# Optimization experiments

Hardware: AMD Instinct MI355X
Metric: run time of the kernel (lower is better)

## Reference

```python
import jax, jax.numpy as jnp
import numpy as np
from jax import lax

B, C, H, W = 4, 256, 64, 64
R = 4  # reduction
BN_EPS = 1e-5


def setup_inputs() -> dict:
    key = jax.random.key(0)
    ks = jax.random.split(key, 18)
    n = jax.random.normal
    return {
        "x_self": n(ks[0], (B, C, H, W), jnp.float32),
        "x_other": n(ks[1], (B, C, H, W), jnp.float32),
        "q_w": n(ks[2], (C, C), jnp.float32) * 0.05,      # self_q 1x1 conv
        "q_b": n(ks[3], (C,), jnp.float32) * 0.05,
        "kv_w": n(ks[4], (2 * C, C), jnp.float32) * 0.05,  # other_kv 1x1 conv
        "kv_b": n(ks[5], (2 * C,), jnp.float32) * 0.05,
        "g1_w": n(ks[6], (C // R, C), jnp.float32) * 0.05,  # gate conv1
        "g1_b": n(ks[7], (C // R,), jnp.float32) * 0.05,
        "g2_w": n(ks[8], (1, C // R), jnp.float32) * 0.05,  # gate conv2
        "g2_b": n(ks[9], (1,), jnp.float32) * 0.05,
        "dw_w": n(ks[10], (C, 1, 3, 3), jnp.float32) * 0.1,  # depthwise 3x3
        "dw_b": n(ks[11], (C,), jnp.float32) * 0.05,
        "bn_g": jnp.ones((C,), jnp.float32),
        "bn_b": jnp.zeros((C,), jnp.float32),
        "bn_m": n(ks[12], (C,), jnp.float32) * 0.05,
        "bn_v": jax.random.uniform(ks[13], (C,), jnp.float32, 0.5, 1.5),
        "out_w": n(ks[14], (C, C), jnp.float32) * 0.05,
        "out_b": n(ks[15], (C,), jnp.float32) * 0.05,
    }


def _conv1x1(x, w, b):
    return jnp.einsum('bchw,oc->bohw', x, w) + b[None, :, None, None]


def reference(x_self, x_other, q_w, q_b, kv_w, kv_b, g1_w, g1_b, g2_w, g2_b,
              dw_w, dw_b, bn_g, bn_b, bn_m, bn_v, out_w, out_b):
    # local branch: depthwise 3x3 conv -> BatchNorm (eval stats) -> SiLU
    y = lax.conv_general_dilated(
        x_self, dw_w, (1, 1), 'SAME',
        feature_group_count=C,
        dimension_numbers=('NCHW', 'OIHW', 'NCHW')) + dw_b[None, :, None, None]
    scale = (bn_g / jnp.sqrt(bn_v + BN_EPS))[None, :, None, None]
    y = (y - bn_m[None, :, None, None]) * scale + bn_b[None, :, None, None]
    local_feat = y * jax.nn.sigmoid(y)  # SiLU

    # cross attention over HW tokens
    q = _conv1x1(x_self, q_w, q_b).reshape(B, C, H * W)
    kv = _conv1x1(x_other, kv_w, kv_b)
    k = kv[:, :C].reshape(B, C, H * W)
    v = kv[:, C:].reshape(B, C, H * W)
    attn = jnp.einsum('bcn,bcm->bnm', q, k) / jnp.sqrt(jnp.float32(C))  # [B,HW,HW]
    attn = jax.nn.softmax(attn, axis=-1)
    attn_out = jnp.einsum('bnm,bcm->bcn', attn, v).reshape(B, C, H, W)

    # channel-squeeze gate on x_self -> scalar per sample
    p = jnp.mean(x_self, axis=(2, 3))                 # [B,C] global avg pool
    g = jax.nn.relu(p @ g1_w.T + g1_b)                # [B,C//R]
    g = jax.nn.sigmoid(g @ g2_w.T + g2_b)             # [B,1]
    gate = g[:, :, None, None]

    fused = local_feat + gate * attn_out
    return _conv1x1(fused, out_w, out_b)
```

## Files before the change

kernel.cpp:

```cpp
#include <hip/hip_runtime.h>
#include <stdint.h>

#define BB 4
#define CC 256
#define HH 64
#define WWD 64
#define NN 4096
#define LOG2E 1.4426950408889634f

typedef __attribute__((ext_vector_type(8))) short short8;
typedef __attribute__((ext_vector_type(4))) float f32x4;
typedef __attribute__((ext_vector_type(16))) float f32x16;
typedef __attribute__((ext_vector_type(4))) unsigned short us4;

__device__ __forceinline__ unsigned short f2bf(float f) {
  unsigned int u = __float_as_uint(f);
  u += 0x7fffu + ((u >> 16) & 1u);
  return (unsigned short)(u >> 16);
}
__device__ __forceinline__ float bf2f(unsigned short h) {
  return __uint_as_float(((unsigned int)h) << 16);
}
__device__ __forceinline__ short8 ld8(const unsigned short* p) {
  return *reinterpret_cast<const short8*>(p);
}
__device__ __forceinline__ int rowmap(int reg, int h) {
  return (reg & 3) + 8 * (reg >> 2) + 4 * h;
}

__global__ __launch_bounds__(256, 2) void k_pre(
    const float* __restrict__ xs, const float* __restrict__ xo,
    const float* __restrict__ dww, const float* __restrict__ dwb,
    const float* __restrict__ bng, const float* __restrict__ bnb,
    const float* __restrict__ bnm, const float* __restrict__ bnv,
    const float* __restrict__ qw, const float* __restrict__ kvw,
    const float* __restrict__ ow, unsigned short* __restrict__ XtS,
    unsigned short* __restrict__ XtO, unsigned short* __restrict__ localT,
    float* __restrict__ psumA, unsigned short* __restrict__ Wb) {
  __shared__ float rb3[3][64][67];
  __shared__ unsigned short sb[64][67];
  int tid = threadIdx.x;
  if (blockIdx.z == 8) {
    int i = (blockIdx.x * 64 + blockIdx.y) * 1024 + tid * 4;
    const float* src;
    if (i < 65536) src = qw + i;
    else if (i < 196608) src = kvw + (i - 65536);
    else src = ow + (i - 196608);
    f32x4 v = *reinterpret_cast<const f32x4*>(src);
    us4 r;
#pragma unroll
    for (int j = 0; j < 4; ++j) r[j] = f2bf(v[j]);
    *reinterpret_cast<us4*>(Wb + i) = r;
    return;
  }
  int c0 = blockIdx.x * 64, h = blockIdx.y;
  int b = blockIdx.z >> 1, which = blockIdx.z & 1;
  const float* src = which ? xo : xs;
  int wq = tid >> 6, w = tid & 63;
  int dlo = which ? 1 : 0, dhi = which ? 1 : 2;
  for (int d = dlo; d <= dhi; ++d) {
    int hh = h + d - 1;
    bool ok = (hh >= 0 && hh < HH);
    for (int p = 0; p < 16; ++p) {
      int cl = p * 4 + wq;
      rb3[d][cl][w + 1] =
          ok ? src[(((size_t)(b * CC + c0 + cl)) * HH + hh) * WWD + w] : 0.f;
    }
    if (tid < 64) { rb3[d][tid][0] = 0.f; rb3[d][tid][65] = 0.f; }
  }
  __syncthreads();
  unsigned short* dst = which ? XtO : XtS;
  int n0 = h * 64, cb = (tid & 15) * 4;
#pragma unroll
  for (int i = 0; i < 4; ++i) {
    int wl = i * 16 + (tid >> 4);
    us4 r;
#pragma unroll
    for (int j = 0; j < 4; ++j) r[j] = f2bf(rb3[1][cb + j][wl + 1]);
    *reinterpret_cast<us4*>(&dst[((size_t)b * NN + n0 + wl) * CC + c0 + cb]) = r;
  }
  if (which) return;
  if (tid < 64) {
    float s = 0.f;
    for (int ww = 0; ww < 64; ++ww) s += rb3[1][tid][ww + 1];
    psumA[((size_t)(b * 64 + h)) * CC + c0 + tid] = s;
  }
  for (int p = 0; p < 16; ++p) {
    int cl = p * 4 + wq, c = c0 + cl;
    float acc = 0.f;
#pragma unroll
    for (int di = 0; di < 3; ++di)
#pragma unroll
      for (int dj = 0; dj < 3; ++dj)
        acc = fmaf(rb3[di][cl][w + dj], dww[c * 9 + di * 3 + dj], acc);
    float y = acc + dwb[c];
    float sc = bng[c] * rsqrtf(bnv[c] + 1e-5f);
    float v = (y - bnm[c]) * sc + bnb[c];
    sb[cl][w] = f2bf(v / (1.f + __expf(-v)));
  }
  __syncthreads();
#pragma unroll
  for (int i = 0; i < 4; ++i) {
    int wl = i * 16 + (tid >> 4);
    us4 r;
#pragma unroll
    for (int j = 0; j < 4; ++j) r[j] = sb[cb + j][wl];
    *reinterpret_cast<us4*>(&localT[((size_t)b * NN + n0 + wl) * CC + c0 + cb]) = r;
  }
}

__global__ __launch_bounds__(256, 4) void k_qkv(
    const unsigned short* __restrict__ XtS, const unsigned short* __restrict__ XtO,
    const unsigned short* __restrict__ Wb, const float* __restrict__ qb,
    const float* __restrict__ kvb, const float* __restrict__ psumA,
    const float* __restrict__ g1w, const float* __restrict__ g1b,
    const float* __restrict__ g2w, const float* __restrict__ g2b,
    unsigned short* __restrict__ Qt, unsigned short* __restrict__ Kt,
    unsigned short* __restrict__ Vv, float* __restrict__ gate) {
  __shared__ unsigned short Xs[64][264];
  int tid = threadIdx.x;
  int id = blockIdx.y;
  if (id == 3) {
    if (blockIdx.x != 0 || blockIdx.z != 0) return;
    float* mf = (float*)&Xs[0][0];
    float* hpf = mf + 1024;
    int c = tid;
    for (int b4 = 0; b4 < 4; ++b4) {
      float s = 0.f;
      for (int hh = 0; hh < 64; ++hh) s += psumA[((size_t)(b4 * 64 + hh)) * CC + c];
      mf[b4 * 256 + c] = s * (1.f / 4096.f);
    }
    __syncthreads();
    for (int b4 = 0; b4 < 4; ++b4) {
      int j = tid >> 2, cq = tid & 3;
      float s = 0.f;
      for (int cc = cq * 64; cc < cq * 64 + 64; ++cc)
        s = fmaf(mf[b4 * 256 + cc], g1w[j * CC + cc], s);
      hpf[j * 5 + cq] = s;
      __syncthreads();
      if (tid < 64) {
        float hh = fmaxf(hpf[tid * 5] + hpf[tid * 5 + 1] + hpf[tid * 5 + 2] +
                             hpf[tid * 5 + 3] + g1b[tid], 0.f);
        float t = hh * g2w[tid];
        for (int off = 32; off; off >>= 1) t += __shfl_down(t, off, 64);
        if (tid == 0) gate[b4] = 1.f / (1.f + expf(-(t + g2b[0])));
      }
      __syncthreads();
    }
    return;
  }
  int n0 = blockIdx.x * 64, b = blockIdx.z;
  const unsigned short* Xt = (id == 0) ? XtS : XtO;
  const unsigned short* W = Wb + id * 65536;
  int wave = tid >> 6, lane = tid & 63, l31 = lane & 31, h = lane >> 5;
#pragma unroll
  for (int p = 0; p < 8; ++p) {
    int r = p * 8 + (tid >> 5), c = (tid & 31) * 8;
    *reinterpret_cast<uint4*>(&Xs[r][c]) =
        *reinterpret_cast<const uint4*>(Xt + ((size_t)b * NN + n0 + r) * CC + c);
  }
  __syncthreads();
  int o0 = wave * 64;
  f32x16 acc[4] = {};
  if (id < 2) {
#pragma unroll
    for (int t = 0; t < 16; ++t) {
      short8 a0 = ld8(&Xs[l31][t * 16 + h * 8]);
      short8 a1 = ld8(&Xs[32 + l31][t * 16 + h * 8]);
      short8 b0 = ld8(W + (size_t)(o0 + l31) * CC + t * 16 + h * 8);
      short8 b1 = ld8(W + (size_t)(o0 + 32 + l31) * CC + t * 16 + h * 8);
      acc[0] = __builtin_amdgcn_mfma_f32_32x32x16_bf16(a0, b0, acc[0], 0, 0, 0);
      acc[1] = __builtin_amdgcn_mfma_f32_32x32x16_bf16(a0, b1, acc[1], 0, 0, 0);
      acc[2] = __builtin_amdgcn_mfma_f32_32x32x16_bf16(a1, b0, acc[2], 0, 0, 0);
      acc[3] = __builtin_amdgcn_mfma_f32_32x32x16_bf16(a1, b1, acc[3], 0, 0, 0);
    }
    const float* bias = id ? kvb : qb;
    unsigned short* Out = id ? Kt : Qt;
    float scale = id ? 1.0f : 0.0625f;
#pragma unroll
    for (int nt = 0; nt < 2; ++nt)
#pragma unroll
      for (int ot = 0; ot < 2; ++ot) {
        int o = o0 + ot * 32 + l31;
        float bv = bias[o];
#pragma unroll
        for (int reg = 0; reg < 16; ++reg) {
          int n = n0 + nt * 32 + rowmap(reg, h);
          Out[((size_t)b * NN + n) * CC + o] = f2bf((acc[nt * 2 + ot][reg] + bv) * scale);
        }
      }
  } else {
#pragma unroll
    for (int t = 0; t < 16; ++t) {
      short8 a0 = ld8(W + (size_t)(o0 + l31) * CC + t * 16 + h * 8);
      short8 a1 = ld8(W + (size_t)(o0 + 32 + l31) * CC + t * 16 + h * 8);
      short8 b0 = ld8(&Xs[l31][t * 16 + h * 8]);
      short8 b1 = ld8(&Xs[32 + l31][t * 16 + h * 8]);
      acc[0] = __builtin_amdgcn_mfma_f32_32x32x16_bf16(a0, b0, acc[0], 0, 0, 0);
      acc[1] = __builtin_amdgcn_mfma_f32_32x32x16_bf16(a0, b1, acc[1], 0, 0, 0);
      acc[2] = __builtin_amdgcn_mfma_f32_32x32x16_bf16(a1, b0, acc[2], 0, 0, 0);
      acc[3] = __builtin_amdgcn_mfma_f32_32x32x16_bf16(a1, b1, acc[3], 0, 0, 0);
    }
#pragma unroll
    for (int ot = 0; ot < 2; ++ot)
#pragma unroll
      for (int nt = 0; nt < 2; ++nt)
#pragma unroll
        for (int reg = 0; reg < 16; ++reg) {
          int o = o0 + ot * 32 + rowmap(reg, h);
          int n = n0 + nt * 32 + l31;
          Vv[((size_t)b * CC + o) * NN + n] = f2bf(acc[ot * 2 + nt][reg] + kvb[CC + o]);
        }
  }
}

__global__ __launch_bounds__(256, 2) void k_flash2(
    const unsigned short* __restrict__ Qt, const unsigned short* __restrict__ Kt,
    const unsigned short* __restrict__ V, const unsigned short* __restrict__ localT,
    const float* __restrict__ gate, float* __restrict__ Opart, float* __restrict__ Lpart,
    unsigned short* __restrict__ fusedT, int iters) {
  __shared__ unsigned short Ks[64][264];
  __shared__ unsigned short Vs[256][72];
  __shared__ unsigned short Ps[64][72];
  __shared__ float lred[2][64];
  __shared__ float ltot[64];
  int b = blockIdx.x & 3, n0 = (blockIdx.x >> 2) * 64;
  int sp = blockIdx.y, nsp = gridDim.y;
  int tid = threadIdx.x, wave = tid >> 6, lane = tid & 63, l31 = lane & 31, h = lane >> 5;
  int rw = wave & 1, cw = wave >> 1;
  const unsigned short* qp = Qt + ((size_t)b * NN + n0 + rw * 32 + l31) * CC + h * 8;
  short8 qf[16];
#pragma unroll
  for (int t = 0; t < 16; ++t) qf[t] = ld8(qp + t * 16);
  f32x16 O[4] = {};
  float lacc[16] = {};
  int mbase = sp * iters * 64;
  for (int it = 0; it < iters; ++it) {
    int m0 = mbase + it * 64;
    __syncthreads();
#pragma unroll
    for (int p = 0; p < 8; ++p) {
      int m = p * 8 + (tid >> 5), ccol = (tid & 31) * 8;
      *reinterpret_cast<uint4*>(&Ks[m][ccol]) =
          *reinterpret_cast<const uint4*>(Kt + ((size_t)b * NN + m0 + m) * CC + ccol);
    }
#pragma unroll
    for (int p = 0; p < 8; ++p) {
      int ccol = p * 32 + (tid >> 3), mm = (tid & 7) * 8;
      *reinterpret_cast<uint4*>(&Vs[ccol][mm]) =
          *reinterpret_cast<const uint4*>(V + ((size_t)b * CC + ccol) * NN + m0 + mm);
    }
    __syncthreads();
    f32x16 S = {};
#pragma unroll
    for (int t = 0; t < 16; ++t) {
      short8 kf = ld8(&Ks[cw * 32 + l31][t * 16 + h * 8]);
      S = __builtin_amdgcn_mfma_f32_32x32x16_bf16(qf[t], kf, S, 0, 0, 0);
    }
#pragma unroll
    for (int reg = 0; reg < 16; ++reg) {
      float p = __builtin_exp2f(S[reg] * LOG2E);
      lacc[reg] += p;
      Ps[rw * 32 + rowmap(reg, h)][cw * 32 + l31] = f2bf(p);
    }
    __syncthreads();
#pragma unroll
    for (int t = 0; t < 4; ++t) {
      short8 pf = ld8(&Ps[rw * 32 + l31][t * 16 + h * 8]);
#pragma unroll
      for (int ct = 0; ct < 4; ++ct) {
        short8 vf = ld8(&Vs[cw * 128 + ct * 32 + l31][t * 16 + h * 8]);
        O[ct] = __builtin_amdgcn_mfma_f32_32x32x16_bf16(pf, vf, O[ct], 0, 0, 0);
      }
    }
  }
#pragma unroll
  for (int reg = 0; reg < 16; ++reg) {
    float v = lacc[reg];
#pragma unroll
    for (int msk = 1; msk < 32; msk <<= 1) v += __shfl_xor(v, msk, 64);
    lacc[reg] = v;
  }
  __syncthreads();
#pragma unroll
  for (int g = 0; g < 16; ++g)
    if (l31 == g) lred[cw][rw * 32 + rowmap(g, h)] = lacc[g];
  __syncthreads();
  size_t obase2 = (size_t)(b * nsp + sp) * NN;
  if (nsp == 1) {
    if (tid < 64) ltot[tid] = lred[0][tid] + lred[1][tid];
    __syncthreads();
    float gv = gate[b];
    float inv[16];
#pragma unroll
    for (int reg = 0; reg < 16; ++reg)
      inv[reg] = gv / ltot[rw * 32 + rowmap(reg, h)];
#pragma unroll
    for (int ct = 0; ct < 4; ++ct)
#pragma unroll
      for (int reg = 0; reg < 16; ++reg) {
        int n = n0 + rw * 32 + rowmap(reg, h);
        int c = cw * 128 + ct * 32 + l31;
        size_t idx = ((size_t)b * NN + n) * CC + c;
        fusedT[idx] = f2bf(bf2f(localT[idx]) + O[ct][reg] * inv[reg]);
      }
  } else {
    if (tid < 64) Lpart[obase2 + n0 + tid] = lred[0][tid] + lred[1][tid];
#pragma unroll
    for (int ct = 0; ct < 4; ++ct)
#pragma unroll
      for (int reg = 0; reg < 16; ++reg) {
        int n = n0 + rw * 32 + rowmap(reg, h);
        int c = cw * 128 + ct * 32 + l31;
        Opart[(obase2 + n) * CC + c] = O[ct][reg];
      }
  }
}

__global__ __launch_bounds__(256, 4) void k_out(
    const unsigned short* __restrict__ W, const float* __restrict__ ob,
    const float* __restrict__ gate, const unsigned short* __restrict__ localT,
    const float* __restrict__ Opart, const float* __restrict__ Lpart,
    const unsigned short* __restrict__ fusedT, float* __restrict__ out, int nsp) {
  __shared__ unsigned short Xs[64][264];
  int n0 = blockIdx.x * 64, o0 = blockIdx.y * 128, b = blockIdx.z;
  int tid = threadIdx.x, wave = tid >> 6, lane = tid & 63, l31 = lane & 31, h = lane >> 5;
  if (Opart) {
    float gv = gate[b];
#pragma unroll
    for (int p = 0; p < 8; ++p) {
      int r = p * 8 + (tid >> 5), cc = (tid & 31) * 8;
      int n = n0 + r;
      float lsum = 0.f;
      for (int sp = 0; sp < nsp; ++sp) lsum += Lpart[(size_t)(b * nsp + sp) * NN + n];
      float g = gv / lsum;
      f32x4 o0v = {}, o1v = {};
      for (int sp = 0; sp < nsp; ++sp) {
        const float* op = &Opart[((size_t)(b * nsp + sp) * NN + n) * CC + cc];
        o0v += *reinterpret_cast<const f32x4*>(op);
        o1v += *reinterpret_cast<const f32x4*>(op + 4);
      }
      const unsigned short* lp = localT + ((size_t)b * NN + n) * CC + cc;
      us4 l0 = *reinterpret_cast<const us4*>(lp), l1 = *reinterpret_cast<const us4*>(lp + 4);
      us4 r0, r1;
#pragma unroll
      for (int j = 0; j < 4; ++j) {
        r0[j] = f2bf(bf2f(l0[j]) + o0v[j] * g);
        r1[j] = f2bf(bf2f(l1[j]) + o1v[j] * g);
      }
      *reinterpret_cast<us4*>(&Xs[r][cc]) = r0;
      *reinterpret_cast<us4*>(&Xs[r][cc + 4]) = r1;
    }
  } else {
#pragma unroll
    for (int p = 0; p < 8; ++p) {
      int r = p * 8 + (tid >> 5), c = (tid & 31) * 8;
      *reinterpret_cast<uint4*>(&Xs[r][c]) =
          *reinterpret_cast<const uint4*>(fusedT + ((size_t)b * NN + n0 + r) * CC + c);
    }
  }
  int obase = o0 + wave * 32;
  short8 af[16];
#pragma unroll
  for (int t = 0; t < 16; ++t) af[t] = ld8(W + (size_t)(obase + l31) * CC + t * 16 + h * 8);
  __syncthreads();
  f32x16 acc[2] = {};
#pragma unroll
  for (int t = 0; t < 16; ++t) {
    short8 b0 = ld8(&Xs[l31][t * 16 + h * 8]);
    short8 b1 = ld8(&Xs[32 + l31][t * 16 + h * 8]);
    acc[0] = __builtin_amdgcn_mfma_f32_32x32x16_bf16(af[t], b0, acc[0], 0, 0, 0);
    acc[1] = __builtin_amdgcn_mfma_f32_32x32x16_bf16(af[t], b1, acc[1], 0, 0, 0);
  }
#pragma unroll
  for (int nt = 0; nt < 2; ++nt)
#pragma unroll
    for (int reg = 0; reg < 16; ++reg) {
      int o = obase + rowmap(reg, h);
      int n = n0 + nt * 32 + l31;
      out[((size_t)b * CC + o) * NN + n] = acc[nt][reg] + ob[o];
    }
}

extern "C" void kernel_launch(void* const* d_in, const int* in_sizes, int n_in,
                              void* d_out, int out_size, void* d_ws, size_t ws_size,
                              hipStream_t stream) {
  const float* xs  = (const float*)d_in[0];
  const float* xo  = (const float*)d_in[1];
  const float* qw  = (const float*)d_in[2];
  const float* qb  = (const float*)d_in[3];
  const float* kvw = (const float*)d_in[4];
  const float* kvb = (const float*)d_in[5];
  const float* g1w = (const float*)d_in[6];
  const float* g1b = (const float*)d_in[7];
  const float* g2w = (const float*)d_in[8];
  const float* g2b = (const float*)d_in[9];
  const float* dww = (const float*)d_in[10];
  const float* dwb = (const float*)d_in[11];
  const float* bng = (const float*)d_in[12];
  const float* bnb = (const float*)d_in[13];
  const float* bnm = (const float*)d_in[14];
  const float* bnv = (const float*)d_in[15];
  const float* ow  = (const float*)d_in[16];
  const float* ob  = (const float*)d_in[17];
  float* out = (float*)d_out;
  char* ws = (char*)d_ws;

  const size_t SZ = (size_t)BB * NN * CC * 2;
  unsigned short* XtS    = (unsigned short*)(ws);
  unsigned short* XtO    = (unsigned short*)(ws + SZ);
  unsigned short* Qt     = (unsigned short*)(ws + 2 * SZ);
  unsigned short* Kt     = (unsigned short*)(ws + 3 * SZ);
  unsigned short* Vv     = (unsigned short*)(ws + 4 * SZ);
  unsigned short* localT = (unsigned short*)(ws + 5 * SZ);
  unsigned short* Wb     = (unsigned short*)(ws + 6 * SZ);
  float* psumA = (float*)(ws + 6 * SZ + 524288);
  float* gate  = (float*)(ws + 6 * SZ + 524288 + 262144);
  size_t tail  = 6 * SZ + 524288 + 262144 + 4096;
  float* Lpart = (float*)(ws + tail);
  float* Opart = (float*)(ws + tail + 131072);
  unsigned short* fusedT = XtS;

  size_t need2 = tail + 131072 + 2ull * 16777216;
  int S = (ws_size >= need2) ? 2 : 1;

  k_pre<<<dim3(4, 64, 9), 256, 0, stream>>>(xs, xo, dww, dwb, bng, bnb, bnm, bnv,
                                            qw, kvw, ow, XtS, XtO, localT, psumA, Wb);
  k_qkv<<<dim3(64, 4, 4), 256, 0, stream>>>(XtS, XtO, Wb, qb, kvb, psumA,
                                            g1w, g1b, g2w, g2b, Qt, Kt, Vv, gate);
  k_flash2<<<dim3(256, S), 256, 0, stream>>>(Qt, Kt, Vv, localT, gate, Opart, Lpart,
                                             fusedT, 64 / S);
  k_out<<<dim3(64, 2, 4), 256, 0, stream>>>(Wb + 196608, ob, gate, localT,
                                            S > 1 ? Opart : nullptr, Lpart, fusedT,
                                            out, S);
}
```

Baseline: 282.8 us.

## Switch attention Q/K/V and P to FP8 MFMA with LDS-staged stores and 3-way split

Q, K, V are now produced as FP8 (with the 1/16 softmax scale split as 0.25 on each of Q and K), staged through shared memory for coalesced 16-byte global stores. The flash kernel uses FP8 32x32x16 MFMAs for both QK^T and PV with byte-sized LDS tiles, and writes bf16 partial outputs. The key split can go to 3 when the workspace allows. The input load in the prologue is also vectorised to float4. The aim is to halve attention memory traffic and speed up the MFMAs. In exchange, FP8 precision on the softmax probabilities and on Q/K/V risks accuracy loss against tolerance.

New measurement: 251.6 us. 11.0% less time.

```diff
diff --git a/kernel.cpp b/kernel.cpp
--- a/kernel.cpp
+++ b/kernel.cpp
@@ -12,6 +12,7 @@
 typedef __attribute__((ext_vector_type(4))) float f32x4;
 typedef __attribute__((ext_vector_type(16))) float f32x16;
 typedef __attribute__((ext_vector_type(4))) unsigned short us4;
+typedef unsigned long long ull;
 
 __device__ __forceinline__ unsigned short f2bf(float f) {
   unsigned int u = __float_as_uint(f);
@@ -23,6 +24,9 @@
 }
 __device__ __forceinline__ short8 ld8(const unsigned short* p) {
   return *reinterpret_cast<const short8*>(p);
+}
+__device__ __forceinline__ unsigned char f2fp8(float v) {
+  return (unsigned char)__builtin_amdgcn_cvt_pk_fp8_f32(v, v, 0, false);
 }
 __device__ __forceinline__ int rowmap(int reg, int h) {
   return (reg & 3) + 8 * (reg >> 2) + 4 * h;
@@ -61,10 +65,16 @@
   for (int d = dlo; d <= dhi; ++d) {
     int hh = h + d - 1;
     bool ok = (hh >= 0 && hh < HH);
-    for (int p = 0; p < 16; ++p) {
-      int cl = p * 4 + wq;
-      rb3[d][cl][w + 1] =
-          ok ? src[(((size_t)(b * CC + c0 + cl)) * HH + hh) * WWD + w] : 0.f;
+#pragma unroll
+    for (int p = 0; p < 4; ++p) {
+      int idx = p * 256 + tid;
+      int cl = idx >> 4, ws4 = (idx & 15) * 4;
+      f32x4 v = {};
+      if (ok)
+        v = *reinterpret_cast<const f32x4*>(
+            &src[(((size_t)(b * CC + c0 + cl)) * HH + hh) * WWD + ws4]);
+#pragma unroll
+      for (int j = 0; j < 4; ++j) rb3[d][cl][ws4 + 1 + j] = v[j];
     }
     if (tid < 64) { rb3[d][tid][0] = 0.f; rb3[d][tid][65] = 0.f; }
   }
@@ -105,7 +115,7 @@
     us4 r;
 #pragma unroll
     for (int j = 0; j < 4; ++j) r[j] = sb[cb + j][wl];
-    *reinterpret_cast<us4*>(&localT[((size_t)b * NN + n0 + wl) * CC + c0 + cb]) = r;
+    *reinterpret_cast<us4*>(&localT[((size_t)b * NN + h * WWD + wl) * CC + c0 + cb]) = r;
   }
 }
 
@@ -115,8 +125,8 @@
     const float* __restrict__ kvb, const float* __restrict__ psumA,
     const float* __restrict__ g1w, const float* __restrict__ g1b,
     const float* __restrict__ g2w, const float* __restrict__ g2b,
-    unsigned short* __restrict__ Qt, unsigned short* __restrict__ Kt,
-    unsigned short* __restrict__ Vv, float* __restrict__ gate) {
+    unsigned char* __restrict__ Qt8, unsigned char* __restrict__ Kt8,
+    unsigned char* __restrict__ Vv8, float* __restrict__ gate) {
   __shared__ unsigned short Xs[64][264];
   int tid = threadIdx.x;
   int id = blockIdx.y;
@@ -175,8 +185,9 @@
       acc[3] = __builtin_amdgcn_mfma_f32_32x32x16_bf16(a1, b1, acc[3], 0, 0, 0);
     }
     const float* bias = id ? kvb : qb;
-    unsigned short* Out = id ? Kt : Qt;
-    float scale = id ? 1.0f : 0.0625f;
+    unsigned char* Out8 = id ? Kt8 : Qt8;
+    __syncthreads();
+    unsigned char (*T8)[264] = reinterpret_cast<unsigned char(*)[264]>(&Xs[0][0]);
 #pragma unroll
     for (int nt = 0; nt < 2; ++nt)
 #pragma unroll
@@ -185,10 +196,21 @@
         float bv = bias[o];
 #pragma unroll
         for (int reg = 0; reg < 16; ++reg) {
-          int n = n0 + nt * 32 + rowmap(reg, h);
-          Out[((size_t)b * NN + n) * CC + o] = f2bf((acc[nt * 2 + ot][reg] + bv) * scale);
+          int nl = nt * 32 + rowmap(reg, h);
+          T8[nl][o] = f2fp8((acc[nt * 2 + ot][reg] + bv) * 0.25f);
         }
       }
+    __syncthreads();
+#pragma unroll
+    for (int p = 0; p < 4; ++p) {
+      int idx = p * 256 + tid, row = idx >> 4, cc = (idx & 15) * 16;
+      ull a0 = *reinterpret_cast<const ull*>(&T8[row][cc]);
+      ull a1 = *reinterpret_cast<const ull*>(&T8[row][cc + 8]);
+      uint4 u;
+      u.x = (unsigned)a0; u.y = (unsigned)(a0 >> 32);
+      u.z = (unsigned)a1; u.w = (unsigned)(a1 >> 32);
+      *reinterpret_cast<uint4*>(Out8 + ((size_t)b * NN + n0 + row) * CC + cc) = u;
+    }
   } else {
 #pragma unroll
     for (int t = 0; t < 16; ++t) {
@@ -201,6 +223,8 @@
       acc[2] = __builtin_amdgcn_mfma_f32_32x32x16_bf16(a1, b0, acc[2], 0, 0, 0);
       acc[3] = __builtin_amdgcn_mfma_f32_32x32x16_bf16(a1, b1, acc[3], 0, 0, 0);
     }
+    __syncthreads();
+    unsigned char (*V8)[72] = reinterpret_cast<unsigned char(*)[72]>(&Xs[0][0]);
 #pragma unroll
     for (int ot = 0; ot < 2; ++ot)
 #pragma unroll
@@ -208,69 +232,84 @@
 #pragma unroll
         for (int reg = 0; reg < 16; ++reg) {
           int o = o0 + ot * 32 + rowmap(reg, h);
-          int n = n0 + nt * 32 + l31;
-          Vv[((size_t)b * CC + o) * NN + n] = f2bf(acc[ot * 2 + nt][reg] + kvb[CC + o]);
+          int nl = nt * 32 + l31;
+          V8[o][nl] = f2fp8(acc[ot * 2 + nt][reg] + kvb[CC + o]);
         }
-  }
-}
-
-__global__ __launch_bounds__(256, 2) void k_flash2(
-    const unsigned short* __restrict__ Qt, const unsigned short* __restrict__ Kt,
-    const unsigned short* __restrict__ V, const unsigned short* __restrict__ localT,
-    const float* __restrict__ gate, float* __restrict__ Opart, float* __restrict__ Lpart,
-    unsigned short* __restrict__ fusedT, int iters) {
-  __shared__ unsigned short Ks[64][264];
-  __shared__ unsigned short Vs[256][72];
-  __shared__ unsigned short Ps[64][72];
+    __syncthreads();
+#pragma unroll
+    for (int p = 0; p < 4; ++p) {
+      int idx = p * 256 + tid, o = idx >> 2, mm = (idx & 3) * 16;
+      ull a0 = *reinterpret_cast<const ull*>(&V8[o][mm]);
+      ull a1 = *reinterpret_cast<const ull*>(&V8[o][mm + 8]);
+      uint4 u;
+      u.x = (unsigned)a0; u.y = (unsigned)(a0 >> 32);
+      u.z = (unsigned)a1; u.w = (unsigned)(a1 >> 32);
+      *reinterpret_cast<uint4*>(Vv8 + ((size_t)b * CC + o) * NN + n0 + mm) = u;
+    }
+  }
+}
+
+__global__ __launch_bounds__(256, 3) void k_flash8(
+    const unsigned char* __restrict__ Qt8, const unsigned char* __restrict__ Kt8,
+    const unsigned char* __restrict__ Vv8, const unsigned short* __restrict__ localT,
+    const float* __restrict__ gate, unsigned short* __restrict__ Opart16,
+    float* __restrict__ Lpart, unsigned short* __restrict__ fusedT) {
+  __shared__ unsigned char Ks8[64][264];
+  __shared__ unsigned char Vs8[256][72];
+  __shared__ unsigned char Ps8[64][72];
   __shared__ float lred[2][64];
   __shared__ float ltot[64];
   int b = blockIdx.x & 3, n0 = (blockIdx.x >> 2) * 64;
   int sp = blockIdx.y, nsp = gridDim.y;
   int tid = threadIdx.x, wave = tid >> 6, lane = tid & 63, l31 = lane & 31, h = lane >> 5;
   int rw = wave & 1, cw = wave >> 1;
-  const unsigned short* qp = Qt + ((size_t)b * NN + n0 + rw * 32 + l31) * CC + h * 8;
-  short8 qf[16];
-#pragma unroll
-  for (int t = 0; t < 16; ++t) qf[t] = ld8(qp + t * 16);
+  const unsigned char* qp = Qt8 + ((size_t)b * NN + n0 + rw * 32 + l31) * CC + h * 8;
+  long qf[16];
+#pragma unroll
+  for (int t = 0; t < 16; ++t) qf[t] = *reinterpret_cast<const long*>(qp + t * 16);
   f32x16 O[4] = {};
   float lacc[16] = {};
-  int mbase = sp * iters * 64;
-  for (int it = 0; it < iters; ++it) {
-    int m0 = mbase + it * 64;
-    __syncthreads();
-#pragma unroll
-    for (int p = 0; p < 8; ++p) {
-      int m = p * 8 + (tid >> 5), ccol = (tid & 31) * 8;
-      *reinterpret_cast<uint4*>(&Ks[m][ccol]) =
-          *reinterpret_cast<const uint4*>(Kt + ((size_t)b * NN + m0 + m) * CC + ccol);
-    }
-#pragma unroll
-    for (int p = 0; p < 8; ++p) {
-      int ccol = p * 32 + (tid >> 3), mm = (tid & 7) * 8;
-      *reinterpret_cast<uint4*>(&Vs[ccol][mm]) =
-          *reinterpret_cast<const uint4*>(V + ((size_t)b * CC + ccol) * NN + m0 + mm);
+  int m_lo = (64 * sp) / nsp, m_hi = (64 * (sp + 1)) / nsp;
+  for (int mt = m_lo; mt < m_hi; ++mt) {
+    int m0 = mt * 64;
+    __syncthreads();
+#pragma unroll
+    for (int p = 0; p < 4; ++p) {
+      int idx = p * 256 + tid, m = idx >> 4, cc = (idx & 15) * 16;
+      const ull* gp = reinterpret_cast<const ull*>(Kt8 + ((size_t)b * NN + m0 + m) * CC + cc);
+      ull a0 = gp[0], a1 = gp[1];
+      *reinterpret_cast<ull*>(&Ks8[m][cc]) = a0;
+      *reinterpret_cast<ull*>(&Ks8[m][cc + 8]) = a1;
+    }
+#pragma unroll
+    for (int p = 0; p < 4; ++p) {
+      int idx = p * 256 + tid, c = idx >> 2, mm = (idx & 3) * 16;
+      const ull* gp = reinterpret_cast<const ull*>(Vv8 + ((size_t)b * CC + c) * NN + m0 + mm);
+      ull a0 = gp[0], a1 = gp[1];
+      *reinterpret_cast<ull*>(&Vs8[c][mm]) = a0;
+      *reinterpret_cast<ull*>(&Vs8[c][mm + 8]) = a1;
     }
     __syncthreads();
     f32x16 S = {};
 #pragma unroll
     for (int t = 0; t < 16; ++t) {
-      short8 kf = ld8(&Ks[cw * 32 + l31][t * 16 + h * 8]);
-      S = __builtin_amdgcn_mfma_f32_32x32x16_bf16(qf[t], kf, S, 0, 0, 0);
+      long kf = *reinterpret_cast<const long*>(&Ks8[cw * 32 + l31][t * 16 + h * 8]);
+      S = __builtin_amdgcn_mfma_f32_32x32x16_fp8_fp8(qf[t], kf, S, 0, 0, 0);
     }
 #pragma unroll
     for (int reg = 0; reg < 16; ++reg) {
       float p = __builtin_exp2f(S[reg] * LOG2E);
       lacc[reg] += p;
-      Ps[rw * 32 + rowmap(reg, h)][cw * 32 + l31] = f2bf(p);
+      Ps8[rw * 32 + rowmap(reg, h)][cw * 32 + l31] = f2fp8(p);
     }
     __syncthreads();
 #pragma unroll
     for (int t = 0; t < 4; ++t) {
-      short8 pf = ld8(&Ps[rw * 32 + l31][t * 16 + h * 8]);
+      long pf = *reinterpret_cast<const long*>(&Ps8[rw * 32 + l31][t * 16 + h * 8]);
 #pragma unroll
       for (int ct = 0; ct < 4; ++ct) {
-        short8 vf = ld8(&Vs[cw * 128 + ct * 32 + l31][t * 16 + h * 8]);
-        O[ct] = __builtin_amdgcn_mfma_f32_32x32x16_bf16(pf, vf, O[ct], 0, 0, 0);
+        long vf = *reinterpret_cast<const long*>(&Vs8[cw * 128 + ct * 32 + l31][t * 16 + h * 8]);
+        O[ct] = __builtin_amdgcn_mfma_f32_32x32x16_fp8_fp8(pf, vf, O[ct], 0, 0, 0);
       }
     }
   }
@@ -312,7 +351,7 @@
       for (int reg = 0; reg < 16; ++reg) {
         int n = n0 + rw * 32 + rowmap(reg, h);
         int c = cw * 128 + ct * 32 + l31;
-        Opart[(obase2 + n) * CC + c] = O[ct][reg];
+        Opart16[(obase2 + n) * CC + c] = f2bf(O[ct][reg]);
       }
   }
 }
@@ -320,12 +359,12 @@
 __global__ __launch_bounds__(256, 4) void k_out(
     const unsigned short* __restrict__ W, const float* __restrict__ ob,
     const float* __restrict__ gate, const unsigned short* __restrict__ localT,
-    const float* __restrict__ Opart, const float* __restrict__ Lpart,
+    const unsigned short* __restrict__ Opart16, const float* __restrict__ Lpart,
     const unsigned short* __restrict__ fusedT, float* __restrict__ out, int nsp) {
   __shared__ unsigned short Xs[64][264];
   int n0 = blockIdx.x * 64, o0 = blockIdx.y * 128, b = blockIdx.z;
   int tid = threadIdx.x, wave = tid >> 6, lane = tid & 63, l31 = lane & 31, h = lane >> 5;
-  if (Opart) {
+  if (Opart16) {
     float gv = gate[b];
 #pragma unroll
     for (int p = 0; p < 8; ++p) {
@@ -334,19 +373,19 @@
       float lsum = 0.f;
       for (int sp = 0; sp < nsp; ++sp) lsum += Lpart[(size_t)(b * nsp + sp) * NN + n];
       float g = gv / lsum;
-      f32x4 o0v = {}, o1v = {};
+      float ov[8] = {};
       for (int sp = 0; sp < nsp; ++sp) {
-        const float* op = &Opart[((size_t)(b * nsp + sp) * NN + n) * CC + cc];
-        o0v += *reinterpret_cast<const f32x4*>(op);
-        o1v += *reinterpret_cast<const f32x4*>(op + 4);
+        short8 x = ld8(Opart16 + ((size_t)(b * nsp + sp) * NN + n) * CC + cc);
+#pragma unroll
+        for (int j = 0; j < 8; ++j) ov[j] += bf2f(((unsigned short*)&x)[j]);
       }
       const unsigned short* lp = localT + ((size_t)b * NN + n) * CC + cc;
-      us4 l0 = *reinterpret_cast<const us4*>(lp), l1 = *reinterpret_cast<const us4*>(lp + 4);
+      short8 lv = ld8(lp);
       us4 r0, r1;
 #pragma unroll
       for (int j = 0; j < 4; ++j) {
-        r0[j] = f2bf(bf2f(l0[j]) + o0v[j] * g);
-        r1[j] = f2bf(bf2f(l1[j]) + o1v[j] * g);
+        r0[j] = f2bf(bf2f(((unsigned short*)&lv)[j]) + ov[j] * g);
+        r1[j] = f2bf(bf2f(((unsigned short*)&lv)[j + 4]) + ov[j + 4] * g);
       }
       *reinterpret_cast<us4*>(&Xs[r][cc]) = r0;
       *reinterpret_cast<us4*>(&Xs[r][cc + 4]) = r1;
@@ -406,31 +445,34 @@
   float* out = (float*)d_out;
   char* ws = (char*)d_ws;
 
-  const size_t SZ = (size_t)BB * NN * CC * 2;
+  const size_t SZ  = (size_t)BB * NN * CC * 2;
+  const size_t SZ8 = (size_t)BB * NN * CC;
   unsigned short* XtS    = (unsigned short*)(ws);
   unsigned short* XtO    = (unsigned short*)(ws + SZ);
-  unsigned short* Qt     = (unsigned short*)(ws + 2 * SZ);
-  unsigned short* Kt     = (unsigned short*)(ws + 3 * SZ);
-  unsigned short* Vv     = (unsigned short*)(ws + 4 * SZ);
-  unsigned short* localT = (unsigned short*)(ws + 5 * SZ);
-  unsigned short* Wb     = (unsigned short*)(ws + 6 * SZ);
-  float* psumA = (float*)(ws + 6 * SZ + 524288);
-  float* gate  = (float*)(ws + 6 * SZ + 524288 + 262144);
-  size_t tail  = 6 * SZ + 524288 + 262144 + 4096;
+  unsigned short* localT = (unsigned short*)(ws + 2 * SZ);
+  unsigned char*  Qt8    = (unsigned char*)(ws + 3 * SZ);
+  unsigned char*  Kt8    = (unsigned char*)(ws + 3 * SZ + SZ8);
+  unsigned char*  Vv8    = (unsigned char*)(ws + 3 * SZ + 2 * SZ8);
+  unsigned short* Wb     = (unsigned short*)(ws + 3 * SZ + 3 * SZ8);
+  float* psumA = (float*)(ws + 3 * SZ + 3 * SZ8 + 524288);
+  float* gate  = (float*)(ws + 3 * SZ + 3 * SZ8 + 524288 + 262144);
+  size_t tail  = 3 * SZ + 3 * SZ8 + 524288 + 262144 + 4096;
   float* Lpart = (float*)(ws + tail);
-  float* Opart = (float*)(ws + tail + 131072);
+  unsigned short* Opart16 = (unsigned short*)(ws + tail + 262144);
   unsigned short* fusedT = XtS;
 
-  size_t need2 = tail + 131072 + 2ull * 16777216;
-  int S = (ws_size >= need2) ? 2 : 1;
+  size_t base = tail + 262144;
+  int S = 1;
+  if (ws_size >= base + 3ull * SZ) S = 3;
+  else if (ws_size >= base + 2ull * SZ) S = 2;
 
   k_pre<<<dim3(4, 64, 9), 256, 0, stream>>>(xs, xo, dww, dwb, bng, bnb, bnm, bnv,
                                             qw, kvw, ow, XtS, XtO, localT, psumA, Wb);
   k_qkv<<<dim3(64, 4, 4), 256, 0, stream>>>(XtS, XtO, Wb, qb, kvb, psumA,
-                                            g1w, g1b, g2w, g2b, Qt, Kt, Vv, gate);
-  k_flash2<<<dim3(256, S), 256, 0, stream>>>(Qt, Kt, Vv, localT, gate, Opart, Lpart,
-                                             fusedT, 64 / S);
+                                            g1w, g1b, g2w, g2b, Qt8, Kt8, Vv8, gate);
+  k_flash8<<<dim3(256, S), 256, 0, stream>>>(Qt8, Kt8, Vv8, localT, gate, Opart16,
+                                             Lpart, fusedT);
   k_out<<<dim3(64, 2, 4), 256, 0, stream>>>(Wb + 196608, ob, gate, localT,
-                                            S > 1 ? Opart : nullptr, Lpart, fusedT,
+                                            S > 1 ? Opart16 : nullptr, Lpart, fusedT,
                                             out, S);
 }
```
